# Kernel optimization log

Hardware: AMD Instinct MI355X
Metric: run time of the kernel (lower is better)

## Reference

```python
import jax, jax.numpy as jnp
import numpy as np

N_NODES = 100000
N_EDGES = 1600000
HIDDEN = 128
IN_CH = 128


def setup_inputs() -> dict:
    key = jax.random.key(0)
    ks = jax.random.split(key, 7)
    x = jax.random.normal(ks[0], (N_NODES, IN_CH), dtype=jnp.float32)
    # edge_index with no self-loops (col != row), matching remove_self_loops
    row = jax.random.randint(ks[1], (N_EDGES,), 0, N_NODES)
    off = jax.random.randint(ks[2], (N_EDGES,), 1, N_NODES)
    col = (row + off) % N_NODES
    edge_index = jnp.stack([row, col], axis=0).astype(jnp.int64)
    Wi = jax.random.normal(ks[3], (HIDDEN, IN_CH), dtype=jnp.float32) * (1.0 / np.sqrt(IN_CH))
    bi = jax.random.normal(ks[4], (HIDDEN,), dtype=jnp.float32) * 0.01
    A = jax.random.normal(ks[5], (HIDDEN, HIDDEN), dtype=jnp.float32) * (1.0 / np.sqrt(HIDDEN))
    Wp = jax.random.normal(ks[6], (HIDDEN, HIDDEN + 2), dtype=jnp.float32) * (1.0 / np.sqrt(HIDDEN))
    return {"x": x, "edge_index": edge_index, "Wi": Wi, "bi": bi, "A": A,
            "Wp": Wp, "num_layers": 4}


def _pairwise_weight(Wp):
    # W0: strictly-upper part symmetrized; diag = q * row-abs-sum + r
    W0 = jnp.triu(Wp[:, :-2], 1)
    W0 = W0 + W0.T
    q = Wp[:, -2]
    r = Wp[:, -1]
    return W0 + jnp.diag(q * jnp.sum(jnp.abs(W0), axis=1) + r)


def reference(x, edge_index, Wi, bi, A, Wp, num_layers):
    n = x.shape[0]
    row, col = edge_index[0], edge_index[1]
    # degree-based symmetric normalization (degree of target nodes)
    deg = jax.ops.segment_sum(jnp.ones_like(col, dtype=x.dtype), col, num_segments=n)
    dinv = jnp.where(deg > 0, jax.lax.rsqrt(jnp.maximum(deg, 1.0)), 0.0)
    norm = dinv[row] * dinv[col]  # [edges]

    Weff = _pairwise_weight(Wp)          # symmetric [H, H]
    Asym = A - A.T                       # antisymmetric [H, H]

    h = jax.nn.relu(x @ Wi.T + bi)       # input projection (dropout eval = id)
    for _ in range(num_layers):
        out = h @ Weff.T                 # symmetric aggr pre-mix
        msg = norm[:, None] * out[row]   # gather + per-edge scale [E, H]
        agg = jax.ops.segment_sum(msg, col, num_segments=n)  # scatter-add
        delta = agg - jax.nn.relu(h @ Asym.T)
        h = h + jax.nn.relu(jnp.tanh(delta))
    return h
```

## Files before the change

### kernel.cpp

```cpp
#include <hip/hip_runtime.h>
#include <hip/hip_bf16.h>

#define HID 128
#define NLAYERS 4
#define SCHUNK 2048
#define WSHIFT 13

typedef __attribute__((ext_vector_type(8))) short bf16x8;
typedef __attribute__((ext_vector_type(4))) float f32x4;

__device__ __forceinline__ float bf2f(unsigned short u) {
    union { unsigned int i; float f; } v; v.i = ((unsigned int)u) << 16; return v.f;
}
__device__ __forceinline__ unsigned short f2bf(float f) {
    union { float f; unsigned int i; } v; v.f = f;
    unsigned int r = v.i + 0x7FFF + ((v.i >> 16) & 1);
    return (unsigned short)(r >> 16);
}

__global__ void k_detect(const unsigned int* ei, int* flag) {
    __shared__ int s;
    if (threadIdx.x == 0) s = 1;
    __syncthreads();
    unsigned int w = ei[threadIdx.x * 2 + 1];
    if (w != 0) s = 0;
    __syncthreads();
    if (threadIdx.x == 0) *flag = s;
}

__global__ void k_convert_edges(const void* ei, const int* flag, int* row32, int* col32,
                                int* deg, int ne) {
    int e = blockIdx.x * blockDim.x + threadIdx.x;
    if (e >= ne) return;
    int r, c;
    if (*flag) {
        const long long* p = (const long long*)ei;
        r = (int)p[e];
        c = (int)p[(size_t)ne + e];
    } else {
        const int* p = (const int*)ei;
        r = p[e];
        c = p[(size_t)ne + e];
    }
    row32[e] = r;
    col32[e] = c;
    atomicAdd(&deg[c], 1);
}

__global__ void k_scan1(const int* deg, int* partial, float* dinv, int n) {
    int tid = threadIdx.x, lane = tid & 63, wid = tid >> 6;
    int i0 = blockIdx.x * SCHUNK + tid * 8;
    int ts = 0;
    #pragma unroll
    for (int j = 0; j < 8; ++j) {
        int i = i0 + j;
        if (i < n) {
            int d = deg[i];
            ts += d;
            dinv[i] = (d > 0) ? rsqrtf((float)d) : 0.f;
        }
    }
    #pragma unroll
    for (int m = 1; m < 64; m <<= 1) ts += __shfl_xor(ts, m);
    __shared__ int ws[4];
    if (lane == 0) ws[wid] = ts;
    __syncthreads();
    if (tid == 0) partial[blockIdx.x] = ws[0] + ws[1] + ws[2] + ws[3];
}

__global__ void k_scan2(int* partial, int nb) {
    int tid = threadIdx.x;
    int v = (tid < nb) ? partial[tid] : 0;
    int s = v;
    #pragma unroll
    for (int off = 1; off < 64; off <<= 1) {
        int t = __shfl_up(s, off);
        if (tid >= off) s += t;
    }
    if (tid < nb) partial[tid] = s - v;
}

__global__ void k_scan3(const int* deg, const int* partial, int* offs, int* pos, int n, int ne) {
    int tid = threadIdx.x, lane = tid & 63, wid = tid >> 6;
    int i0 = blockIdx.x * SCHUNK + tid * 8;
    int v[8], ts = 0;
    #pragma unroll
    for (int j = 0; j < 8; ++j) { v[j] = (i0 + j < n) ? deg[i0 + j] : 0; ts += v[j]; }
    int s = ts;
    #pragma unroll
    for (int off = 1; off < 64; off <<= 1) { int t = __shfl_up(s, off); if (lane >= off) s += t; }
    __shared__ int ws[4];
    if (lane == 63) ws[wid] = s;
    __syncthreads();
    int run = partial[blockIdx.x] + (s - ts);
    for (int w = 0; w < wid; ++w) run += ws[w];
    #pragma unroll
    for (int j = 0; j < 8; ++j) {
        if (i0 + j < n) { offs[i0 + j] = run; pos[i0 + j] = run; }
        run += v[j];
    }
    if (blockIdx.x == 0 && tid == 0) offs[n] = ne;
}

__global__ void k_csrfill(const int* row32, const int* col32, int* pos, int* csr,
                          int ne, int nwin) {
    int cls = blockIdx.x & 7;
    int slice = blockIdx.x >> 3;
    int e0 = (slice * blockDim.x + threadIdx.x) * 4;
    int r[4], c[4], w[4];
    #pragma unroll
    for (int k = 0; k < 4; ++k) {
        int e = e0 + k;
        if (e < ne) { c[k] = col32[e]; r[k] = row32[e]; w[k] = c[k] >> WSHIFT; }
        else w[k] = -1;
    }
    for (int p = cls; p < nwin; p += 8) {
        #pragma unroll
        for (int k = 0; k < 4; ++k) {
            if (w[k] == p) {
                int q = atomicAdd(&pos[c[k]], 1);
                csr[q] = r[k];
            }
        }
    }
}

__global__ void k_weff(const float* Wp, unsigned short* WeffB) {
    int i = blockIdx.x, j = threadIdx.x;
    float w = (i < j) ? Wp[i * 130 + j] : ((i > j) ? Wp[j * 130 + i] : 0.f);
    float a = fabsf(w);
    #pragma unroll
    for (int m = 1; m < 64; m <<= 1) a += __shfl_xor(a, m);
    __shared__ float ws[2];
    if ((j & 63) == 0) ws[j >> 6] = a;
    __syncthreads();
    float rs = ws[0] + ws[1];
    if (i == j) w = Wp[i * 130 + 128] * rs + Wp[i * 130 + 129];
    WeffB[i * 128 + j] = f2bf(w);
}

__global__ void k_asym_wi(const float* A, const float* Wi, unsigned short* AsymB, unsigned short* WiB) {
    int idx = blockIdx.x * blockDim.x + threadIdx.x;
    if (idx >= 16384) return;
    int i = idx >> 7, j = idx & 127;
    AsymB[idx] = f2bf(A[idx] - A[j * 128 + i]);
    WiB[idx] = f2bf(Wi[idx]);
}

__launch_bounds__(256, 2)
__global__ void k_gemm0(const float* x, const unsigned short* WiB, const float* bi,
                        const float* dinv, float* h, unsigned short* hb,
                        unsigned short* hsb, int n) {
    int wid = threadIdx.x >> 6, lane = threadIdx.x & 63;
    int row0 = blockIdx.x * 64 + wid * 16;
    int lrow = lane & 15, lk = (lane >> 4) * 8;
    int arow = row0 + lrow; if (arow >= n) arow = n - 1;
    const float* Aptr = x + (size_t)arow * 128;
    f32x4 acc[8];
    #pragma unroll
    for (int cf = 0; cf < 8; ++cf) acc[cf] = (f32x4)(0.f);
    #pragma unroll
    for (int kk = 0; kk < 4; ++kk) {
        float4 xa = *(const float4*)(Aptr + kk * 32 + lk);
        float4 xc = *(const float4*)(Aptr + kk * 32 + lk + 4);
        bf16x8 a;
        a[0] = (short)f2bf(xa.x); a[1] = (short)f2bf(xa.y);
        a[2] = (short)f2bf(xa.z); a[3] = (short)f2bf(xa.w);
        a[4] = (short)f2bf(xc.x); a[5] = (short)f2bf(xc.y);
        a[6] = (short)f2bf(xc.z); a[7] = (short)f2bf(xc.w);
        #pragma unroll
        for (int cf = 0; cf < 8; ++cf) {
            bf16x8 b = *(const bf16x8*)(WiB + (size_t)(cf * 16 + lrow) * 128 + kk * 32 + lk);
            acc[cf] = __builtin_amdgcn_mfma_f32_16x16x32_bf16(a, b, acc[cf], 0, 0, 0);
        }
    }
    int orow_base = row0 + (lane >> 4) * 4;
    #pragma unroll
    for (int r = 0; r < 4; ++r) {
        int orow = orow_base + r;
        if (orow >= n) continue;
        float dv = dinv[orow];
        #pragma unroll
        for (int cf = 0; cf < 8; ++cf) {
            int col = cf * 16 + lrow;
            float v = acc[cf][r] + bi[col];
            v = fmaxf(v, 0.f);
            h[(size_t)orow * 128 + col] = v;
            hb[(size_t)orow * 128 + col] = f2bf(v);
            hsb[(size_t)orow * 128 + col] = f2bf(v * dv);
        }
    }
}

__launch_bounds__(256, 8)
__global__ void k_gather(const unsigned short* hsb, const int* csr, const int* offs,
                         unsigned short* aggHb, int n) {
    int wid = threadIdx.x >> 6, lane = threadIdx.x & 63;
    int c = blockIdx.x * 4 + wid;
    if (c >= n) return;
    int g = lane >> 4;
    int fl = lane & 15;
    int s = offs[c], e = offs[c + 1];
    float accA[8], accB[8];
    #pragma unroll
    for (int k = 0; k < 8; ++k) { accA[k] = 0.f; accB[k] = 0.f; }
    int j = s;
    for (; j + 16 <= e; j += 16) {
        int r0 = csr[j + g];
        int r1 = csr[j + 4 + g];
        int r2 = csr[j + 8 + g];
        int r3 = csr[j + 12 + g];
        uint4 v0 = *(const uint4*)(hsb + (size_t)r0 * 128 + fl * 8);
        uint4 v1 = *(const uint4*)(hsb + (size_t)r1 * 128 + fl * 8);
        uint4 v2 = *(const uint4*)(hsb + (size_t)r2 * 128 + fl * 8);
        uint4 v3 = *(const uint4*)(hsb + (size_t)r3 * 128 + fl * 8);
        accA[0] += bf2f((unsigned short)(v0.x & 0xffff)); accA[1] += bf2f((unsigned short)(v0.x >> 16));
        accA[2] += bf2f((unsigned short)(v0.y & 0xffff)); accA[3] += bf2f((unsigned short)(v0.y >> 16));
        accA[4] += bf2f((unsigned short)(v0.z & 0xffff)); accA[5] += bf2f((unsigned short)(v0.z >> 16));
        accA[6] += bf2f((unsigned short)(v0.w & 0xffff)); accA[7] += bf2f((unsigned short)(v0.w >> 16));
        accB[0] += bf2f((unsigned short)(v1.x & 0xffff)); accB[1] += bf2f((unsigned short)(v1.x >> 16));
        accB[2] += bf2f((unsigned short)(v1.y & 0xffff)); accB[3] += bf2f((unsigned short)(v1.y >> 16));
        accB[4] += bf2f((unsigned short)(v1.z & 0xffff)); accB[5] += bf2f((unsigned short)(v1.z >> 16));
        accB[6] += bf2f((unsigned short)(v1.w & 0xffff)); accB[7] += bf2f((unsigned short)(v1.w >> 16));
        accA[0] += bf2f((unsigned short)(v2.x & 0xffff)); accA[1] += bf2f((unsigned short)(v2.x >> 16));
        accA[2] += bf2f((unsigned short)(v2.y & 0xffff)); accA[3] += bf2f((unsigned short)(v2.y >> 16));
        accA[4] += bf2f((unsigned short)(v2.z & 0xffff)); accA[5] += bf2f((unsigned short)(v2.z >> 16));
        accA[6] += bf2f((unsigned short)(v2.w & 0xffff)); accA[7] += bf2f((unsigned short)(v2.w >> 16));
        accB[0] += bf2f((unsigned short)(v3.x & 0xffff)); accB[1] += bf2f((unsigned short)(v3.x >> 16));
        accB[2] += bf2f((unsigned short)(v3.y & 0xffff)); accB[3] += bf2f((unsigned short)(v3.y >> 16));
        accB[4] += bf2f((unsigned short)(v3.z & 0xffff)); accB[5] += bf2f((unsigned short)(v3.z >> 16));
        accB[6] += bf2f((unsigned short)(v3.w & 0xffff)); accB[7] += bf2f((unsigned short)(v3.w >> 16));
    }
    for (; j < e; j += 8) {
        int i0 = j + g, i1 = j + 4 + g;
        if (i0 < e) {
            int r = csr[i0];
            uint4 v = *(const uint4*)(hsb + (size_t)r * 128 + fl * 8);
            accA[0] += bf2f((unsigned short)(v.x & 0xffff)); accA[1] += bf2f((unsigned short)(v.x >> 16));
            accA[2] += bf2f((unsigned short)(v.y & 0xffff)); accA[3] += bf2f((unsigned short)(v.y >> 16));
            accA[4] += bf2f((unsigned short)(v.z & 0xffff)); accA[5] += bf2f((unsigned short)(v.z >> 16));
            accA[6] += bf2f((unsigned short)(v.w & 0xffff)); accA[7] += bf2f((unsigned short)(v.w >> 16));
        }
        if (i1 < e) {
            int r = csr[i1];
            uint4 v = *(const uint4*)(hsb + (size_t)r * 128 + fl * 8);
            accB[0] += bf2f((unsigned short)(v.x & 0xffff)); accB[1] += bf2f((unsigned short)(v.x >> 16));
            accB[2] += bf2f((unsigned short)(v.y & 0xffff)); accB[3] += bf2f((unsigned short)(v.y >> 16));
            accB[4] += bf2f((unsigned short)(v.z & 0xffff)); accB[5] += bf2f((unsigned short)(v.z >> 16));
            accB[6] += bf2f((unsigned short)(v.w & 0xffff)); accB[7] += bf2f((unsigned short)(v.w >> 16));
        }
    }
    #pragma unroll
    for (int k = 0; k < 8; ++k) {
        float a = accA[k] + accB[k];
        a += __shfl_xor(a, 16);
        a += __shfl_xor(a, 32);
        accA[k] = a;
    }
    int f0 = fl * 8 + g * 2;
    unsigned int o = ((unsigned int)f2bf(accA[g * 2 + 1]) << 16) | (unsigned int)f2bf(accA[g * 2]);
    *(unsigned int*)(aggHb + (size_t)c * 128 + f0) = o;
}

__launch_bounds__(256, 2)
__global__ void k_gemm_upd(const unsigned short* aggHb, const unsigned short* WeffB,
                           const unsigned short* AsymB, const float* dinv,
                           float* h, unsigned short* hb, unsigned short* hsb, int n) {
    int wid = threadIdx.x >> 6, lane = threadIdx.x & 63;
    int row0 = blockIdx.x * 64 + wid * 16;
    int lrow = lane & 15, lk = (lane >> 4) * 8;
    int arow = row0 + lrow; if (arow >= n) arow = n - 1;
    const bf16x8* Ag = (const bf16x8*)(aggHb + (size_t)arow * 128);
    const bf16x8* Ah = (const bf16x8*)(hb + (size_t)arow * 128);
    f32x4 acc0[8], acc1[8];
    #pragma unroll
    for (int cf = 0; cf < 8; ++cf) { acc0[cf] = (f32x4)(0.f); acc1[cf] = (f32x4)(0.f); }
    #pragma unroll
    for (int kk = 0; kk < 4; ++kk) {
        bf16x8 ag = Ag[kk * 4 + (lk >> 3)];
        bf16x8 ah = Ah[kk * 4 + (lk >> 3)];
        #pragma unroll
        for (int cf = 0; cf < 8; ++cf) {
            bf16x8 b0 = *(const bf16x8*)(WeffB + (size_t)(cf * 16 + lrow) * 128 + kk * 32 + lk);
            acc0[cf] = __builtin_amdgcn_mfma_f32_16x16x32_bf16(ag, b0, acc0[cf], 0, 0, 0);
            bf16x8 b1 = *(const bf16x8*)(AsymB + (size_t)(cf * 16 + lrow) * 128 + kk * 32 + lk);
            acc1[cf] = __builtin_amdgcn_mfma_f32_16x16x32_bf16(ah, b1, acc1[cf], 0, 0, 0);
        }
    }
    int orow_base = row0 + (lane >> 4) * 4;
    #pragma unroll
    for (int r = 0; r < 4; ++r) {
        int orow = orow_base + r;
        if (orow >= n) continue;
        float dv = dinv[orow];
        #pragma unroll
        for (int cf = 0; cf < 8; ++cf) {
            int col = cf * 16 + lrow;
            float delta = dv * acc0[cf][r] - fmaxf(acc1[cf][r], 0.f);
            float u = fmaxf(tanhf(delta), 0.f);
            size_t idx = (size_t)orow * 128 + col;
            float hv = h[idx] + u;
            h[idx] = hv;
            hb[idx] = f2bf(hv);
            hsb[idx] = f2bf(hv * dv);
        }
    }
}

extern "C" void kernel_launch(void* const* d_in, const int* in_sizes, int n_in,
                              void* d_out, int out_size, void* d_ws, size_t ws_size,
                              hipStream_t stream) {
    const float* x  = (const float*)d_in[0];
    const void*  ei = d_in[1];
    const float* Wi = (const float*)d_in[2];
    const float* bi = (const float*)d_in[3];
    const float* A  = (const float*)d_in[4];
    const float* Wp = (const float*)d_in[5];

    const int n  = in_sizes[0] / HID;
    const int ne = in_sizes[1] / 2;

    char* w = (char*)d_ws;
    size_t o = 0;
    auto alloc = [&](size_t bytes) -> void* {
        void* p = w + o;
        o = (o + bytes + 255) & ~(size_t)255;
        return p;
    };
    int*            flag    = (int*)alloc(4);
    int*            row32   = (int*)alloc((size_t)ne * 4);
    int*            col32   = (int*)alloc((size_t)ne * 4);
    int*            deg     = (int*)alloc((size_t)n * 4);
    float*          dinv    = (float*)alloc((size_t)n * 4);
    int*            offs    = (int*)alloc((size_t)(n + 1) * 4);
    int*            pos     = (int*)alloc((size_t)n * 4);
    int*            partial = (int*)alloc(64 * 4);
    int*            csr     = (int*)alloc((size_t)ne * 4);
    unsigned short* WeffB   = (unsigned short*)alloc(16384 * 2);
    unsigned short* AsymB   = (unsigned short*)alloc(16384 * 2);
    unsigned short* WiB     = (unsigned short*)alloc(16384 * 2);
    unsigned short* hb      = (unsigned short*)alloc((size_t)n * 128 * 2);
    unsigned short* hsb     = (unsigned short*)alloc((size_t)n * 128 * 2);
    unsigned short* aggHb   = (unsigned short*)alloc((size_t)n * 128 * 2);
    if (o > ws_size) return;

    float* h = (float*)d_out;

    hipMemsetAsync(deg, 0, (size_t)n * 4, stream);

    int eb = (ne + 255) / 256;
    int sb = (n + SCHUNK - 1) / SCHUNK;
    int nwin = (n + (1 << WSHIFT) - 1) >> WSHIFT;

    k_detect<<<1, 256, 0, stream>>>((const unsigned int*)ei, flag);
    k_convert_edges<<<eb, 256, 0, stream>>>(ei, flag, row32, col32, deg, ne);
    k_scan1<<<sb, 256, 0, stream>>>(deg, partial, dinv, n);
    k_scan2<<<1, 64, 0, stream>>>(partial, sb);
    k_scan3<<<sb, 256, 0, stream>>>(deg, partial, offs, pos, n, ne);
    int fb = (ne + 1023) / 1024;
    k_csrfill<<<fb * 8, 256, 0, stream>>>(row32, col32, pos, csr, ne, nwin);
    k_weff<<<128, 128, 0, stream>>>(Wp, WeffB);
    k_asym_wi<<<64, 256, 0, stream>>>(A, Wi, AsymB, WiB);

    int gb = (n + 63) / 64;
    k_gemm0<<<gb, 256, 0, stream>>>(x, WiB, bi, dinv, h, hb, hsb, n);

    int ab = (n + 3) / 4;
    for (int l = 0; l < NLAYERS; ++l) {
        k_gather<<<ab, 256, 0, stream>>>(hsb, csr, offs, aggHb, n);
        k_gemm_upd<<<gb, 256, 0, stream>>>(aggHb, WeffB, AsymB, dinv, h, hb, hsb, n);
    }
}
```

Measured before the change: 827.8 us.

## Drop bf16 h copy and split update GEMMs across waves via LDS

Removes the separate bf16 copy of h: the Asym GEMM now reads fp32 h and converts it to bf16 in registers. This saves one 2-byte-per-element write per layer and in the input projection. The update kernel now handles 32 rows per block. Two waves compute the Weff product and two compute the Asym product, exchanging ReLU(h·Asym) through shared memory, which halves accumulator registers and allows higher occupancy. The cost is an extra fp32 read of h, a block barrier, and half of the waves sitting idle during the epilogue.

```diff
diff --git a/kernel.cpp b/kernel.cpp
--- a/kernel.cpp
+++ b/kernel.cpp
@@ -149,8 +149,7 @@
 
 __launch_bounds__(256, 2)
 __global__ void k_gemm0(const float* x, const unsigned short* WiB, const float* bi,
-                        const float* dinv, float* h, unsigned short* hb,
-                        unsigned short* hsb, int n) {
+                        const float* dinv, float* h, unsigned short* hsb, int n) {
     int wid = threadIdx.x >> 6, lane = threadIdx.x & 63;
     int row0 = blockIdx.x * 64 + wid * 16;
     int lrow = lane & 15, lk = (lane >> 4) * 8;
@@ -186,7 +185,6 @@
             float v = acc[cf][r] + bi[col];
             v = fmaxf(v, 0.f);
             h[(size_t)orow * 128 + col] = v;
-            hb[(size_t)orow * 128 + col] = f2bf(v);
             hsb[(size_t)orow * 128 + col] = f2bf(v * dv);
         }
     }
@@ -262,47 +260,74 @@
     *(unsigned int*)(aggHb + (size_t)c * 128 + f0) = o;
 }
 
-__launch_bounds__(256, 2)
+__launch_bounds__(256, 4)
 __global__ void k_gemm_upd(const unsigned short* aggHb, const unsigned short* WeffB,
                            const unsigned short* AsymB, const float* dinv,
-                           float* h, unsigned short* hb, unsigned short* hsb, int n) {
-    int wid = threadIdx.x >> 6, lane = threadIdx.x & 63;
-    int row0 = blockIdx.x * 64 + wid * 16;
+                           float* h, unsigned short* hsb, int n) {
+    __shared__ float zl[32][132];
+    int wv = threadIdx.x >> 6, lane = threadIdx.x & 63;
+    int t = wv & 1;
+    int m = wv >> 1;
+    int row0 = blockIdx.x * 32 + t * 16;
     int lrow = lane & 15, lk = (lane >> 4) * 8;
     int arow = row0 + lrow; if (arow >= n) arow = n - 1;
-    const bf16x8* Ag = (const bf16x8*)(aggHb + (size_t)arow * 128);
-    const bf16x8* Ah = (const bf16x8*)(hb + (size_t)arow * 128);
-    f32x4 acc0[8], acc1[8];
-    #pragma unroll
-    for (int cf = 0; cf < 8; ++cf) { acc0[cf] = (f32x4)(0.f); acc1[cf] = (f32x4)(0.f); }
-    #pragma unroll
-    for (int kk = 0; kk < 4; ++kk) {
-        bf16x8 ag = Ag[kk * 4 + (lk >> 3)];
-        bf16x8 ah = Ah[kk * 4 + (lk >> 3)];
-        #pragma unroll
-        for (int cf = 0; cf < 8; ++cf) {
-            bf16x8 b0 = *(const bf16x8*)(WeffB + (size_t)(cf * 16 + lrow) * 128 + kk * 32 + lk);
-            acc0[cf] = __builtin_amdgcn_mfma_f32_16x16x32_bf16(ag, b0, acc0[cf], 0, 0, 0);
-            bf16x8 b1 = *(const bf16x8*)(AsymB + (size_t)(cf * 16 + lrow) * 128 + kk * 32 + lk);
-            acc1[cf] = __builtin_amdgcn_mfma_f32_16x16x32_bf16(ah, b1, acc1[cf], 0, 0, 0);
-        }
-    }
-    int orow_base = row0 + (lane >> 4) * 4;
-    #pragma unroll
-    for (int r = 0; r < 4; ++r) {
-        int orow = orow_base + r;
-        if (orow >= n) continue;
-        float dv = dinv[orow];
-        #pragma unroll
-        for (int cf = 0; cf < 8; ++cf) {
-            int col = cf * 16 + lrow;
-            float delta = dv * acc0[cf][r] - fmaxf(acc1[cf][r], 0.f);
-            float u = fmaxf(tanhf(delta), 0.f);
-            size_t idx = (size_t)orow * 128 + col;
-            float hv = h[idx] + u;
-            h[idx] = hv;
-            hb[idx] = f2bf(hv);
-            hsb[idx] = f2bf(hv * dv);
+    f32x4 acc[8];
+    #pragma unroll
+    for (int cf = 0; cf < 8; ++cf) acc[cf] = (f32x4)(0.f);
+    if (m == 1) {
+        const float* Ap = h + (size_t)arow * 128;
+        #pragma unroll
+        for (int kk = 0; kk < 4; ++kk) {
+            float4 xa = *(const float4*)(Ap + kk * 32 + lk);
+            float4 xc = *(const float4*)(Ap + kk * 32 + lk + 4);
+            bf16x8 a;
+            a[0] = (short)f2bf(xa.x); a[1] = (short)f2bf(xa.y);
+            a[2] = (short)f2bf(xa.z); a[3] = (short)f2bf(xa.w);
+            a[4] = (short)f2bf(xc.x); a[5] = (short)f2bf(xc.y);
+            a[6] = (short)f2bf(xc.z); a[7] = (short)f2bf(xc.w);
+            #pragma unroll
+            for (int cf = 0; cf < 8; ++cf) {
+                bf16x8 b = *(const bf16x8*)(AsymB + (size_t)(cf * 16 + lrow) * 128 + kk * 32 + lk);
+                acc[cf] = __builtin_amdgcn_mfma_f32_16x16x32_bf16(a, b, acc[cf], 0, 0, 0);
+            }
+        }
+        int lr0 = t * 16 + (lane >> 4) * 4;
+        #pragma unroll
+        for (int r = 0; r < 4; ++r)
+            #pragma unroll
+            for (int cf = 0; cf < 8; ++cf)
+                zl[lr0 + r][cf * 16 + lrow] = fmaxf(acc[cf][r], 0.f);
+    } else {
+        const bf16x8* Ap = (const bf16x8*)(aggHb + (size_t)arow * 128);
+        #pragma unroll
+        for (int kk = 0; kk < 4; ++kk) {
+            bf16x8 a = Ap[kk * 4 + (lk >> 3)];
+            #pragma unroll
+            for (int cf = 0; cf < 8; ++cf) {
+                bf16x8 b = *(const bf16x8*)(WeffB + (size_t)(cf * 16 + lrow) * 128 + kk * 32 + lk);
+                acc[cf] = __builtin_amdgcn_mfma_f32_16x16x32_bf16(a, b, acc[cf], 0, 0, 0);
+            }
+        }
+    }
+    __syncthreads();
+    if (m == 0) {
+        int orow_base = row0 + (lane >> 4) * 4;
+        int lr0 = t * 16 + (lane >> 4) * 4;
+        #pragma unroll
+        for (int r = 0; r < 4; ++r) {
+            int orow = orow_base + r;
+            if (orow >= n) continue;
+            float dv = dinv[orow];
+            #pragma unroll
+            for (int cf = 0; cf < 8; ++cf) {
+                int col = cf * 16 + lrow;
+                float delta = dv * acc[cf][r] - zl[lr0 + r][col];
+                float u = fmaxf(tanhf(delta), 0.f);
+                size_t idx = (size_t)orow * 128 + col;
+                float hv = h[idx] + u;
+                h[idx] = hv;
+                hsb[idx] = f2bf(hv * dv);
+            }
         }
     }
 }
@@ -339,7 +364,6 @@
     unsigned short* WeffB   = (unsigned short*)alloc(16384 * 2);
     unsigned short* AsymB   = (unsigned short*)alloc(16384 * 2);
     unsigned short* WiB     = (unsigned short*)alloc(16384 * 2);
-    unsigned short* hb      = (unsigned short*)alloc((size_t)n * 128 * 2);
     unsigned short* hsb     = (unsigned short*)alloc((size_t)n * 128 * 2);
     unsigned short* aggHb   = (unsigned short*)alloc((size_t)n * 128 * 2);
     if (o > ws_size) return;
@@ -363,11 +387,12 @@
     k_asym_wi<<<64, 256, 0, stream>>>(A, Wi, AsymB, WiB);
 
     int gb = (n + 63) / 64;
-    k_gemm0<<<gb, 256, 0, stream>>>(x, WiB, bi, dinv, h, hb, hsb, n);
+    k_gemm0<<<gb, 256, 0, stream>>>(x, WiB, bi, dinv, h, hsb, n);
 
     int ab = (n + 3) / 4;
+    int ub = (n + 31) / 32;
     for (int l = 0; l < NLAYERS; ++l) {
         k_gather<<<ab, 256, 0, stream>>>(hsb, csr, offs, aggHb, n);
-        k_gemm_upd<<<gb, 256, 0, stream>>>(aggHb, WeffB, AsymB, dinv, h, hb, hsb, n);
-    }
-}
+        k_gemm_upd<<<ub, 256, 0, stream>>>(aggHb, WeffB, AsymB, dinv, h, hsb, n);
+    }
+}
```

After: 747.5 us. 9.7% less time.
